# Kernel optimization log

Hardware: AMD Instinct MI355X
Metric: run time of the kernel (lower is better)

The kernel has to match this reference:

```python
import jax, jax.numpy as jnp
import numpy as np

N_COMBIN, N_DEV, CONT, VOCAB, EMB = 50000, 100000, 62, 1000, 16
B, K, H, OUT, NCLS = 8192, 64, 4, 16, 1
FEAT = CONT + 2 * EMB  # 94
ALPHA = 0.2  # leaky relu slope


def setup_inputs() -> dict:
    key = jax.random.key(0)
    ks = jax.random.split(key, 32)
    rn = lambda k, shape, s=0.05: (jax.random.normal(k, shape, dtype=jnp.float32) * s)
    inp = {
        "combin_cont": jax.random.normal(ks[0], (N_COMBIN, CONT), jnp.float32),
        "combin_cat": jax.random.randint(ks[1], (N_COMBIN, 2), 0, VOCAB),
        "device_cont": jax.random.normal(ks[2], (N_DEV, CONT), jnp.float32),
        "device_cat": jax.random.randint(ks[3], (N_DEV, 2), 0, VOCAB),
        "combin_idx": jax.random.randint(ks[4], (B,), 0, N_COMBIN),
        "device_idx": jax.random.randint(ks[5], (B,), 0, N_DEV),
        "neighbor_idx": jax.random.randint(ks[6], (B, K), 0, N_DEV),
        "ce0": rn(ks[7], (VOCAB, EMB), 1.0),
        "ce1": rn(ks[8], (VOCAB, EMB), 1.0),
        "de0": rn(ks[9], (VOCAB, EMB), 1.0),
        "de1": rn(ks[10], (VOCAB, EMB), 1.0),
        "Wc": rn(ks[11], (H, FEAT, OUT)),
        "bc": rn(ks[12], (H, OUT)),
        "Wd": rn(ks[13], (H, FEAT, OUT)),
        "bd": rn(ks[14], (H, OUT)),
        "aW": rn(ks[15], (H, 2 * OUT)),
        "ab": rn(ks[16], (H,)),
        "W1": rn(ks[17], (H * OUT, OUT)),
        "b1": rn(ks[18], (OUT,)),
        "W2": rn(ks[19], (OUT + 2 * FEAT, 64)),
        "b2": rn(ks[20], (64,)),
        "W3": rn(ks[21], (64, 32)),
        "b3": rn(ks[22], (32,)),
        "W4": rn(ks[23], (32, NCLS)),
        "b4": rn(ks[24], (NCLS,)),
    }
    return inp


def reference(combin_cont, combin_cat, device_cont, device_cat,
              combin_idx, device_idx, neighbor_idx,
              ce0, ce1, de0, de1,
              Wc, bc, Wd, bd, aW, ab,
              W1, b1, W2, b2, W3, b3, W4, b4):
    # concat_embed_feats for device nodes: [N_dev, FEAT]
    dev_feats = jnp.concatenate(
        [device_cont, de0[device_cat[:, 0]], de1[device_cat[:, 1]]], axis=1)
    # combin batch features: [B, FEAT]
    cc = combin_cat[combin_idx]
    comb_batch = jnp.concatenate(
        [combin_cont[combin_idx], ce0[cc[:, 0]], ce1[cc[:, 1]]], axis=1)
    dev_batch = dev_feats[device_idx]            # [B, FEAT]
    neibr = dev_feats[neighbor_idx]              # [B, K, FEAT]

    # multi-head GAT attention (all heads vectorized)
    h_c = jnp.einsum('bf,hfo->bho', comb_batch, Wc) + bc[None]          # [B,H,OUT]
    h_n = jnp.einsum('bkf,hfo->bhko', neibr, Wd) + bd[None, :, None]    # [B,H,K,OUT]
    a1, a2 = aW[:, :OUT], aW[:, OUT:]
    e = (jnp.einsum('bho,ho->bh', h_c, a1)[:, :, None]
         + jnp.einsum('bhko,ho->bhk', h_n, a2)
         + ab[None, :, None])                                           # [B,H,K]
    e = jax.nn.leaky_relu(e, negative_slope=ALPHA)
    attn = jax.nn.softmax(e, axis=-1)
    head_out = jax.nn.elu(jnp.einsum('bhk,bhko->bho', attn, h_n))       # [B,H,OUT]
    attn_feats = head_out.reshape(head_out.shape[0], H * OUT) @ W1 + b1  # [B,OUT]

    fusion = jnp.concatenate([comb_batch, dev_batch, attn_feats], axis=1)
    x = jax.nn.relu(fusion @ W2 + b2)   # dropout is identity in eval
    x = jax.nn.relu(x @ W3 + b3)
    return jax.nn.sigmoid(x @ W4 + b4)  # [B, NCLS]
```

## Files before the change

kernel.cpp:

```cpp
#include <hip/hip_runtime.h>
#include <cmath>

#define NDEV   100000
#define NBATCH 8192
#define CONTF  62
#define EMB    16
#define FEAT   94
#define KNBR   64
#define NH     4
#define OUTD   16
#define HOUT   64
#define FUS    204
#define ALPHA  0.2f

#define NDEVG  1563
#define NCOMBG 128
#define KP     48

typedef unsigned short ushortT;
typedef unsigned int   uintT;
typedef ushortT ushort8v __attribute__((ext_vector_type(8)));
typedef short   short8  __attribute__((ext_vector_type(8)));
typedef float   float4v __attribute__((ext_vector_type(4)));


template <typename T>
__device__ __forceinline__ const T* uniform_ptr(const T* p) {
  uint64_t v = (uint64_t)(uintptr_t)p;
  uint32_t lo = __builtin_amdgcn_readfirstlane((uint32_t)v);
  uint32_t hi = __builtin_amdgcn_readfirstlane((uint32_t)(v >> 32));
  return (const T*)(uintptr_t)(((uint64_t)hi << 32) | lo);
}

__device__ __forceinline__ float bf2f(ushortT u) {
  return __uint_as_float(((unsigned int)u) << 16);
}
__device__ __forceinline__ ushortT f2bf(float f) {
  unsigned int i = __float_as_uint(f);
  unsigned int r = i + 0x7FFFu + ((i >> 16) & 1u);
  return (ushortT)(r >> 16);
}
__device__ __forceinline__ uintT pack2(float lo, float hi) {
  return ((uintT)f2bf(hi) << 16) | (uintT)f2bf(lo);
}

union FragU { uint4 u; short8 s; };

__global__ __launch_bounds__(256) void k_prep(
    const float* __restrict__ Wd, const float* __restrict__ Wc,
    uintT* __restrict__ wpack) {
  const int e = blockIdx.x * 256 + threadIdx.x;
  if (e >= 2 * 64 * KP) return;
  const bool dev = e < 64 * KP;
  const int i = dev ? e : e - 64 * KP;
  const int n = i / KP, p = i - n * KP;
  const int h = n >> 4, o = n & 15;
  const float* __restrict__ Ws = dev ? Wd : Wc;
  uintT v = 0u;
  if (p < 47) {
    const float lo = Ws[(h * FEAT + 2 * p) * OUTD + o];
    const float hi = Ws[(h * FEAT + 2 * p + 1) * OUTD + o];
    v = pack2(lo, hi);
  }
  wpack[e] = v;
}

__global__ __launch_bounds__(256, 2) void k_feat(
    const float* __restrict__ device_cont, const int* __restrict__ device_cat,
    const float* __restrict__ de0, const float* __restrict__ de1,
    const float* __restrict__ bd,
    const float* __restrict__ combin_cont, const int* __restrict__ combin_cat,
    const int* __restrict__ combin_idx,
    const float* __restrict__ ce0, const float* __restrict__ ce1,
    const float* __restrict__ bc,
    const float* __restrict__ aW, const uintT* __restrict__ wpack,
    ushortT* __restrict__ h_bf, float* __restrict__ e_d, float* __restrict__ e_c) {
  __shared__ uintT x_s[64 * KP];
  __shared__ uintT w_s[64 * KP];
  __shared__ int   ci_s[64];

  const int tid  = threadIdx.x;
  const int lane = tid & 63;
  const int wv = __builtin_amdgcn_readfirstlane((int)(tid >> 6));
  const int blk = blockIdx.x;
  const bool devp = blk < NDEVG;
  const int b0 = (devp ? blk : blk - NDEVG) * 64;

  if (!devp && tid < 64) ci_s[tid] = combin_idx[b0 + tid];

  {
    const uint4* __restrict__ wp =
        reinterpret_cast<const uint4*>(wpack + (devp ? 0 : 64 * KP));
#pragma unroll
    for (int t = 0; t < 3; ++t)
      reinterpret_cast<uint4*>(w_s)[t * 256 + tid] = wp[t * 256 + tid];
  }
  __syncthreads();

  {
    const float* __restrict__ cont = devp ? device_cont : combin_cont;
#pragma unroll 1
    for (int e = tid; e < 64 * 31; e += 256) {
      const int r = e / 31, p = e - r * 31;
      const size_t srow = devp ? (size_t)min(b0 + r, NDEV - 1) : (size_t)ci_s[r];
      const float2 v = *reinterpret_cast<const float2*>(cont + srow * CONTF + 2 * p);
      x_s[r * KP + p] = pack2(v.x, v.y);
    }
  }
  if (tid < 128) {
    const int r = tid >> 1, tb = tid & 1;
    const int srow = devp ? min(b0 + r, NDEV - 1) : ci_s[r];
    const int cidx = (devp ? device_cat : combin_cat)[2 * srow + tb];
    const float* __restrict__ ep =
        (tb ? (devp ? de1 : ce1) : (devp ? de0 : ce0)) + (size_t)cidx * EMB;
    uintT* __restrict__ dst = &x_s[r * KP + 31 + tb * 8];
#pragma unroll
    for (int k4 = 0; k4 < 4; ++k4) {
      const float4 v = reinterpret_cast<const float4*>(ep)[k4];
      dst[2 * k4 + 0] = pack2(v.x, v.y);
      dst[2 * k4 + 1] = pack2(v.z, v.w);
    }
  }
  if (tid < 64) x_s[tid * KP + 47] = 0u;
  __syncthreads();

  const int m = lane & 15, q = lane >> 4;
  const float* bias = uniform_ptr(devp ? bd : bc);
  const float* aWl  = uniform_ptr(aW);

  float4v acc[NH];
#pragma unroll
  for (int ct = 0; ct < NH; ++ct) {
    const float bv = bias[ct * OUTD + m];
    acc[ct] = (float4v){bv, bv, bv, bv};
  }

  const uintT* xa = &x_s[(wv * 16 + m) * KP + q * 4];
#pragma unroll
  for (int c = 0; c < 3; ++c) {
    FragU af;
    af.u = *reinterpret_cast<const uint4*>(xa + c * 16);
#pragma unroll
    for (int ct = 0; ct < NH; ++ct) {
      FragU bf;
      bf.u = *reinterpret_cast<const uint4*>(&w_s[(ct * 16 + m) * KP + c * 16 + q * 4]);
      acc[ct] = __builtin_amdgcn_mfma_f32_16x16x32_bf16(af.s, bf.s, acc[ct], 0, 0, 0);
    }
  }

  const int aoff = devp ? OUTD : 0;
  float* __restrict__ eout = devp ? e_d : e_c;
#pragma unroll
  for (int ct = 0; ct < NH; ++ct) {
    const float av = aWl[ct * 2 * OUTD + aoff + m];
    float e0 = acc[ct][0] * av, e1 = acc[ct][1] * av,
          e2 = acc[ct][2] * av, e3 = acc[ct][3] * av;
#pragma unroll
    for (int msk = 1; msk < 16; msk <<= 1) {
      e0 += __shfl_xor(e0, msk);
      e1 += __shfl_xor(e1, msk);
      e2 += __shfl_xor(e2, msk);
      e3 += __shfl_xor(e3, msk);
    }
    if (m == ct) {
      const int row = b0 + wv * 16 + q * 4;
      const float ev[4] = {e0, e1, e2, e3};
#pragma unroll
      for (int r = 0; r < 4; ++r)
        if (!devp || row + r < NDEV) eout[(size_t)(row + r) * NH + ct] = ev[r];
    }
  }
  if (devp) {
#pragma unroll
    for (int ct = 0; ct < NH; ++ct) {
#pragma unroll
      for (int r = 0; r < 4; ++r) {
        const int row = b0 + wv * 16 + q * 4 + r;
        if (row < NDEV)
          h_bf[(size_t)row * HOUT + ct * OUTD + m] = f2bf(acc[ct][r]);
      }
    }
  }
}

__global__ __launch_bounds__(256, 4) void k_attn(
    const int* __restrict__ neighbor_idx, const int* __restrict__ device_idx,
    const int* __restrict__ device_cat, const float* __restrict__ device_cont,
    const float* __restrict__ de0, const float* __restrict__ de1,
    const int* __restrict__ combin_idx, const int* __restrict__ combin_cat,
    const float* __restrict__ combin_cont,
    const float* __restrict__ ce0, const float* __restrict__ ce1,
    const ushortT* __restrict__ h_bf, const float* __restrict__ e_d,
    const float* __restrict__ e_c, const float* __restrict__ ab,
    const float* __restrict__ W1, const float* __restrict__ b1,
    const float* __restrict__ W2, const float* __restrict__ b2,
    const float* __restrict__ W3, const float* __restrict__ b3,
    const float* __restrict__ W4, const float* __restrict__ b4,
    float* __restrict__ out) {
  __shared__ __align__(16) float pb[4][NH][68];
  __shared__ __align__(16) int   nb[4][KNBR];
  __shared__ __align__(16) float hb[4][HOUT];
  __shared__ __align__(16) float fusb[4][208];
  __shared__ __align__(16) float x1b[4][64];

  const int lane = threadIdx.x & 63;
  const int wid  = __builtin_amdgcn_readfirstlane((int)(threadIdx.x >> 6));
  const int b    = blockIdx.x * 4 + wid;

  const int nk = neighbor_idx[(size_t)b * KNBR + lane];
  const float4 ed4 = *reinterpret_cast<const float4*>(e_d + (size_t)nk * NH);
  const float4 ec4 = *reinterpret_cast<const float4*>(e_c + (size_t)b * NH);
  const float4 ab4 = *reinterpret_cast<const float4*>(ab);

  float v0 = ec4.x + ed4.x + ab4.x;
  float v1 = ec4.y + ed4.y + ab4.y;
  float v2 = ec4.z + ed4.z + ab4.z;
  float v3 = ec4.w + ed4.w + ab4.w;
  v0 = v0 > 0.f ? v0 : ALPHA * v0;
  v1 = v1 > 0.f ? v1 : ALPHA * v1;
  v2 = v2 > 0.f ? v2 : ALPHA * v2;
  v3 = v3 > 0.f ? v3 : ALPHA * v3;

  float m0 = v0, m1 = v1, m2 = v2, m3 = v3;
#pragma unroll
  for (int msk = 1; msk < 64; msk <<= 1) {
    m0 = fmaxf(m0, __shfl_xor(m0, msk));
    m1 = fmaxf(m1, __shfl_xor(m1, msk));
    m2 = fmaxf(m2, __shfl_xor(m2, msk));
    m3 = fmaxf(m3, __shfl_xor(m3, msk));
  }
  float p0 = expf(v0 - m0), p1 = expf(v1 - m1), p2 = expf(v2 - m2), p3 = expf(v3 - m3);
  float s0 = p0, s1 = p1, s2 = p2, s3 = p3;
#pragma unroll
  for (int msk = 1; msk < 64; msk <<= 1) {
    s0 += __shfl_xor(s0, msk);
    s1 += __shfl_xor(s1, msk);
    s2 += __shfl_xor(s2, msk);
    s3 += __shfl_xor(s3, msk);
  }
  p0 /= s0; p1 /= s1; p2 /= s2; p3 /= s3;

  pb[wid][0][lane] = p0;
  pb[wid][1][lane] = p1;
  pb[wid][2][lane] = p2;
  pb[wid][3][lane] = p3;
  nb[wid][lane]    = nk;

  const int ci = combin_idx[b];
  const int cc0 = combin_cat[2 * ci], cc1 = combin_cat[2 * ci + 1];
  const int didx = device_idx[b];
  const int dc0 = device_cat[2 * didx], dc1 = device_cat[2 * didx + 1];
#pragma unroll
  for (int t = 0; t < 3; ++t) {
    const int i = lane + t * 64;
    if (i < 188) {
      float v;
      if (i < 62)       v = combin_cont[(size_t)ci * CONTF + i];
      else if (i < 78)  v = ce0[(size_t)cc0 * EMB + (i - 62)];
      else if (i < 94)  v = ce1[(size_t)cc1 * EMB + (i - 78)];
      else if (i < 156) v = device_cont[(size_t)didx * CONTF + (i - 94)];
      else if (i < 172) v = de0[(size_t)dc0 * EMB + (i - 156)];
      else              v = de1[(size_t)dc1 * EMB + (i - 172)];
      fusb[wid][i] = v;
    }
  }
  __syncthreads();

  {
    const int q = lane >> 3, c8 = lane & 7;
    const int hq = c8 >> 1;
    float a[8];
#pragma unroll
    for (int i = 0; i < 8; ++i) a[i] = 0.f;
#pragma unroll
    for (int t = 0; t < 8; ++t) {
      const int k   = q * 8 + t;
      const int n   = nb[wid][k];
      const float p = pb[wid][hq][k];
      const ushort8v hv =
          *reinterpret_cast<const ushort8v*>(h_bf + (size_t)n * HOUT + c8 * 8);
#pragma unroll
      for (int i = 0; i < 8; ++i) a[i] = fmaf(p, bf2f(hv[i]), a[i]);
    }
#pragma unroll
    for (int msk = 8; msk < 64; msk <<= 1) {
#pragma unroll
      for (int i = 0; i < 8; ++i) a[i] += __shfl_xor(a[i], msk);
    }
    if (q == 0) {
#pragma unroll
      for (int i = 0; i < 8; ++i) a[i] = a[i] > 0.f ? a[i] : expm1f(a[i]);
      float4* hp = reinterpret_cast<float4*>(&hb[wid][c8 * 8]);
      hp[0] = make_float4(a[0], a[1], a[2], a[3]);
      hp[1] = make_float4(a[4], a[5], a[6], a[7]);
    }
  }
  __syncthreads();

  {
    const int j = lane & 15, gg = lane >> 4;
    float part = 0.f;
#pragma unroll
    for (int t = 0; t < 16; ++t)
      part = fmaf(hb[wid][gg * 16 + t], W1[(gg * 16 + t) * OUTD + j], part);
    part += __shfl_xor(part, 16);
    part += __shfl_xor(part, 32);
    if (lane < 16) fusb[wid][188 + lane] = part + b1[lane];
  }
  __syncthreads();

  float acc = b2[lane];
#pragma unroll 4
  for (int f = 0; f < FUS; ++f)
    acc = fmaf(fusb[wid][f], W2[f * 64 + lane], acc);
  x1b[wid][lane] = fmaxf(acc, 0.f);

  const int m = lane & 31, rh = lane >> 5;
  float x2 = rh ? 0.f : b3[m];
#pragma unroll 4
  for (int j = 0; j < 32; ++j) {
    const int jj = rh * 32 + j;
    x2 = fmaf(x1b[wid][jj], W3[jj * 32 + m], x2);
  }
  x2 += __shfl_xor(x2, 32);
  float pL3 = fmaxf(x2, 0.f) * W4[m];
#pragma unroll
  for (int msk = 1; msk < 32; msk <<= 1) pL3 += __shfl_xor(pL3, msk);
  if (lane == 0) {
    const float z = pL3 + b4[0];
    out[b] = 1.f / (1.f + expf(-z));
  }
}

extern "C" void kernel_launch(void* const* d_in, const int* in_sizes, int n_in,
                              void* d_out, int out_size, void* d_ws, size_t ws_size,
                              hipStream_t stream) {
  const float* combin_cont  = (const float*)d_in[0];
  const int*   combin_cat   = (const int*)d_in[1];
  const float* device_cont  = (const float*)d_in[2];
  const int*   device_cat   = (const int*)d_in[3];
  const int*   combin_idx   = (const int*)d_in[4];
  const int*   device_idx   = (const int*)d_in[5];
  const int*   neighbor_idx = (const int*)d_in[6];
  const float* ce0 = (const float*)d_in[7];
  const float* ce1 = (const float*)d_in[8];
  const float* de0 = (const float*)d_in[9];
  const float* de1 = (const float*)d_in[10];
  const float* Wc  = (const float*)d_in[11];
  const float* bc  = (const float*)d_in[12];
  const float* Wd  = (const float*)d_in[13];
  const float* bd  = (const float*)d_in[14];
  const float* aW  = (const float*)d_in[15];
  const float* ab  = (const float*)d_in[16];
  const float* W1  = (const float*)d_in[17];
  const float* b1  = (const float*)d_in[18];
  const float* W2  = (const float*)d_in[19];
  const float* b2  = (const float*)d_in[20];
  const float* W3  = (const float*)d_in[21];
  const float* b3  = (const float*)d_in[22];
  const float* W4  = (const float*)d_in[23];
  const float* b4  = (const float*)d_in[24];

  float* ws  = (float*)d_ws;
  ushortT* h_bf = (ushortT*)ws;
  float* e_d = ws + 3200000;
  float* e_c = ws + 3600000;
  uintT* wpack = (uintT*)(ws + 3632768);

  k_prep<<<24, 256, 0, stream>>>(Wd, Wc, wpack);
  k_feat<<<NDEVG + NCOMBG, 256, 0, stream>>>(
      device_cont, device_cat, de0, de1, bd,
      combin_cont, combin_cat, combin_idx, ce0, ce1, bc, aW, wpack,
      h_bf, e_d, e_c);
  k_attn<<<2048, 256, 0, stream>>>(
      neighbor_idx, device_idx, device_cat, device_cont, de0, de1,
      combin_idx, combin_cat, combin_cont, ce0, ce1,
      h_bf, e_d, e_c, ab, W1, b1, W2, b2, W3, b3, W4, b4, (float*)d_out);
}
```

Before: 167.0 us.

## Process 128 rows per k_feat block and use wave barriers in k_attn

```diff
diff --git a/kernel.cpp b/kernel.cpp
--- a/kernel.cpp
+++ b/kernel.cpp
@@ -13,9 +13,9 @@
 #define FUS    204
 #define ALPHA  0.2f
 
-#define NDEVG  1563
-#define NCOMBG 128
-#define KP     48
+#define NDEVG2  782
+#define NCOMBG2 64
+#define KP      48
 
 typedef unsigned short ushortT;
 typedef unsigned int   uintT;
@@ -75,18 +75,18 @@
     const float* __restrict__ bc,
     const float* __restrict__ aW, const uintT* __restrict__ wpack,
     ushortT* __restrict__ h_bf, float* __restrict__ e_d, float* __restrict__ e_c) {
-  __shared__ uintT x_s[64 * KP];
+  __shared__ uintT x_s[128 * KP];
   __shared__ uintT w_s[64 * KP];
-  __shared__ int   ci_s[64];
+  __shared__ int   ci_s[128];
 
   const int tid  = threadIdx.x;
   const int lane = tid & 63;
   const int wv = __builtin_amdgcn_readfirstlane((int)(tid >> 6));
   const int blk = blockIdx.x;
-  const bool devp = blk < NDEVG;
-  const int b0 = (devp ? blk : blk - NDEVG) * 64;
-
-  if (!devp && tid < 64) ci_s[tid] = combin_idx[b0 + tid];
+  const bool devp = blk < NDEVG2;
+  const int b0 = (devp ? blk : blk - NDEVG2) * 128;
+
+  if (!devp && tid < 128) ci_s[tid] = combin_idx[b0 + tid];
 
   {
     const uint4* __restrict__ wp =
@@ -100,14 +100,14 @@
   {
     const float* __restrict__ cont = devp ? device_cont : combin_cont;
 #pragma unroll 1
-    for (int e = tid; e < 64 * 31; e += 256) {
+    for (int e = tid; e < 128 * 31; e += 256) {
       const int r = e / 31, p = e - r * 31;
       const size_t srow = devp ? (size_t)min(b0 + r, NDEV - 1) : (size_t)ci_s[r];
       const float2 v = *reinterpret_cast<const float2*>(cont + srow * CONTF + 2 * p);
       x_s[r * KP + p] = pack2(v.x, v.y);
     }
   }
-  if (tid < 128) {
+  {
     const int r = tid >> 1, tb = tid & 1;
     const int srow = devp ? min(b0 + r, NDEV - 1) : ci_s[r];
     const int cidx = (devp ? device_cat : combin_cat)[2 * srow + tb];
@@ -121,63 +121,69 @@
       dst[2 * k4 + 1] = pack2(v.z, v.w);
     }
   }
-  if (tid < 64) x_s[tid * KP + 47] = 0u;
+  if (tid < 128) x_s[tid * KP + 47] = 0u;
   __syncthreads();
 
   const int m = lane & 15, q = lane >> 4;
   const float* bias = uniform_ptr(devp ? bd : bc);
   const float* aWl  = uniform_ptr(aW);
 
-  float4v acc[NH];
+  float4v acc[2][NH];
 #pragma unroll
   for (int ct = 0; ct < NH; ++ct) {
     const float bv = bias[ct * OUTD + m];
-    acc[ct] = (float4v){bv, bv, bv, bv};
-  }
-
-  const uintT* xa = &x_s[(wv * 16 + m) * KP + q * 4];
+    acc[0][ct] = (float4v){bv, bv, bv, bv};
+    acc[1][ct] = (float4v){bv, bv, bv, bv};
+  }
+
+  const uintT* xa0 = &x_s[(wv * 16 + m) * KP + q * 4];
+  const uintT* xa1 = &x_s[(64 + wv * 16 + m) * KP + q * 4];
 #pragma unroll
   for (int c = 0; c < 3; ++c) {
-    FragU af;
-    af.u = *reinterpret_cast<const uint4*>(xa + c * 16);
+    FragU af0, af1;
+    af0.u = *reinterpret_cast<const uint4*>(xa0 + c * 16);
+    af1.u = *reinterpret_cast<const uint4*>(xa1 + c * 16);
 #pragma unroll
     for (int ct = 0; ct < NH; ++ct) {
       FragU bf;
       bf.u = *reinterpret_cast<const uint4*>(&w_s[(ct * 16 + m) * KP + c * 16 + q * 4]);
-      acc[ct] = __builtin_amdgcn_mfma_f32_16x16x32_bf16(af.s, bf.s, acc[ct], 0, 0, 0);
+      acc[0][ct] = __builtin_amdgcn_mfma_f32_16x16x32_bf16(af0.s, bf.s, acc[0][ct], 0, 0, 0);
+      acc[1][ct] = __builtin_amdgcn_mfma_f32_16x16x32_bf16(af1.s, bf.s, acc[1][ct], 0, 0, 0);
     }
   }
 
   const int aoff = devp ? OUTD : 0;
   float* __restrict__ eout = devp ? e_d : e_c;
 #pragma unroll
-  for (int ct = 0; ct < NH; ++ct) {
-    const float av = aWl[ct * 2 * OUTD + aoff + m];
-    float e0 = acc[ct][0] * av, e1 = acc[ct][1] * av,
-          e2 = acc[ct][2] * av, e3 = acc[ct][3] * av;
-#pragma unroll
-    for (int msk = 1; msk < 16; msk <<= 1) {
-      e0 += __shfl_xor(e0, msk);
-      e1 += __shfl_xor(e1, msk);
-      e2 += __shfl_xor(e2, msk);
-      e3 += __shfl_xor(e3, msk);
-    }
-    if (m == ct) {
-      const int row = b0 + wv * 16 + q * 4;
-      const float ev[4] = {e0, e1, e2, e3};
-#pragma unroll
-      for (int r = 0; r < 4; ++r)
-        if (!devp || row + r < NDEV) eout[(size_t)(row + r) * NH + ct] = ev[r];
-    }
-  }
-  if (devp) {
+  for (int rt = 0; rt < 2; ++rt) {
+    const int rowq = b0 + rt * 64 + wv * 16 + q * 4;
 #pragma unroll
     for (int ct = 0; ct < NH; ++ct) {
-#pragma unroll
-      for (int r = 0; r < 4; ++r) {
-        const int row = b0 + wv * 16 + q * 4 + r;
-        if (row < NDEV)
-          h_bf[(size_t)row * HOUT + ct * OUTD + m] = f2bf(acc[ct][r]);
+      const float av = aWl[ct * 2 * OUTD + aoff + m];
+      float e0 = acc[rt][ct][0] * av, e1 = acc[rt][ct][1] * av,
+            e2 = acc[rt][ct][2] * av, e3 = acc[rt][ct][3] * av;
+#pragma unroll
+      for (int msk = 1; msk < 16; msk <<= 1) {
+        e0 += __shfl_xor(e0, msk);
+        e1 += __shfl_xor(e1, msk);
+        e2 += __shfl_xor(e2, msk);
+        e3 += __shfl_xor(e3, msk);
+      }
+      if (m == ct) {
+        const float ev[4] = {e0, e1, e2, e3};
+#pragma unroll
+        for (int r = 0; r < 4; ++r)
+          if (!devp || rowq + r < NDEV) eout[(size_t)(rowq + r) * NH + ct] = ev[r];
+      }
+    }
+    if (devp) {
+#pragma unroll
+      for (int ct = 0; ct < NH; ++ct) {
+#pragma unroll
+        for (int r = 0; r < 4; ++r) {
+          if (rowq + r < NDEV)
+            h_bf[(size_t)(rowq + r) * HOUT + ct * OUTD + m] = f2bf(acc[rt][ct][r]);
+        }
       }
     }
   }
@@ -264,7 +270,7 @@
       fusb[wid][i] = v;
     }
   }
-  __syncthreads();
+  __builtin_amdgcn_wave_barrier();
 
   {
     const int q = lane >> 3, c8 = lane & 7;
@@ -295,7 +301,7 @@
       hp[1] = make_float4(a[4], a[5], a[6], a[7]);
     }
   }
-  __syncthreads();
+  __builtin_amdgcn_wave_barrier();
 
   {
     const int j = lane & 15, gg = lane >> 4;
@@ -307,13 +313,14 @@
     part += __shfl_xor(part, 32);
     if (lane < 16) fusb[wid][188 + lane] = part + b1[lane];
   }
-  __syncthreads();
+  __builtin_amdgcn_wave_barrier();
 
   float acc = b2[lane];
 #pragma unroll 4
   for (int f = 0; f < FUS; ++f)
     acc = fmaf(fusb[wid][f], W2[f * 64 + lane], acc);
   x1b[wid][lane] = fmaxf(acc, 0.f);
+  __builtin_amdgcn_wave_barrier();
 
   const int m = lane & 31, rh = lane >> 5;
   float x2 = rh ? 0.f : b3[m];
@@ -368,7 +375,7 @@
   uintT* wpack = (uintT*)(ws + 3632768);
 
   k_prep<<<24, 256, 0, stream>>>(Wd, Wc, wpack);
-  k_feat<<<NDEVG + NCOMBG, 256, 0, stream>>>(
+  k_feat<<<NDEVG2 + NCOMBG2, 256, 0, stream>>>(
       device_cont, device_cat, de0, de1, bd,
       combin_cont, combin_cat, combin_idx, ce0, ce1, bc, aW, wpack,
       h_bf, e_d, e_c);
```

Result: no change. 165.9 us (-0.6%).
